# Kernel tuning notes

Hardware: AMD Instinct MI355X
Metric: run time of the kernel (lower is better)

## Reference

```python
import jax, jax.numpy as jnp
import numpy as np

N_NODES = 50000
N_EDGES = 1250000
D_FEAT = 64


def setup_inputs() -> dict:
    key = jax.random.key(0)
    k1, k2, k3, k4 = jax.random.split(key, 4)
    feat = jax.random.normal(k1, (N_NODES, D_FEAT), dtype=jnp.float32)
    edge_weight = jax.random.uniform(k2, (N_EDGES,), dtype=jnp.float32)
    edge_src = jax.random.randint(k3, (N_EDGES,), 0, N_NODES, dtype=jnp.int64)
    edge_dst = jnp.sort(jax.random.randint(k4, (N_EDGES,), 0, N_NODES, dtype=jnp.int64))
    return {"feat": feat, "edge_weight": edge_weight,
            "edge_src": edge_src, "edge_dst": edge_dst}


def reference(feat, edge_weight, edge_src, edge_dst):
    # u_mul_e: gather source node features, scale by per-edge weight
    msgs = feat[edge_src] * edge_weight[:, None]          # [E, d]
    # fn.sum: scatter-add messages to destination nodes
    rst = jax.ops.segment_sum(msgs, edge_dst, num_segments=N_NODES)  # [N, d]
    return rst
```

## Files before the change

kernel.cpp:

```cpp
#include <hip/hip_runtime.h>
#include <hip/hip_fp16.h>

#define D_FEAT 64

__global__ __launch_bounds__(256) void prep_kernel(
    const float* __restrict__ feat, uint2* __restrict__ f16,
    const int* __restrict__ edge_dst, int* __restrict__ rp,
    int n_vec4, int n_edges, int n_nodes, int rb) {
  if ((int)blockIdx.x < rb) {
    const int i = blockIdx.x * blockDim.x + threadIdx.x;
    if (i >= n_vec4) return;
    const float4 v = ((const float4*)feat)[i];
    const __half2 h0 = __float22half2_rn(make_float2(v.x, v.y));
    const __half2 h1 = __float22half2_rn(make_float2(v.z, v.w));
    uint2 o;
    o.x = *(const unsigned int*)&h0;
    o.y = *(const unsigned int*)&h1;
    f16[i] = o;
  } else {
    const int e = (blockIdx.x - rb) * blockDim.x + threadIdx.x;
    if (e > n_edges) return;
    const int d0 = (e == 0) ? -1 : edge_dst[e - 1];
    const int d1 = (e == n_edges) ? n_nodes : edge_dst[e];
    for (int v = d0 + 1; v <= d1; ++v) rp[v] = e;
  }
}

__global__ __launch_bounds__(256) void gcn_gather_f16(
    const uint4* __restrict__ feat16,
    const float* __restrict__ ew,
    const int* __restrict__ esrc,
    const int* __restrict__ rp,
    float* __restrict__ out, int n_nodes) {
  const int total16 = n_nodes * 8;
  const int warm_slices = (total16 + 1023) / 1024;
  const int xcd_seq = blockIdx.x >> 3;
  if (xcd_seq < warm_slices) {
    const int s0 = xcd_seq * 1024;
#pragma unroll
    for (int t = 0; t < 4; ++t) {
      const int idx = s0 + t * 256 + threadIdx.x;
      if (idx < total16) {
        uint4 q = feat16[idx];
        asm volatile("" :: "v"(q.x), "v"(q.y), "v"(q.z), "v"(q.w));
      }
    }
  }

  const int wave = (blockIdx.x * blockDim.x + threadIdx.x) >> 6;
  const int lane = threadIdx.x & 63;
  if (wave >= n_nodes) return;
  const int slot = lane >> 3;
  const int part = lane & 7;

  const int e0 = rp[wave];
  const int e1 = rp[wave + 1];

  float a0 = 0.f, a1 = 0.f, a2 = 0.f, a3 = 0.f;
  float a4 = 0.f, a5 = 0.f, a6 = 0.f, a7 = 0.f;

  for (int base = e0; base < e1; base += 64) {
    const int n = min(64, e1 - base);
    int   s = 0;
    float w = 0.0f;
    if (lane < n) {
      s = esrc[base + lane];
      w = ew[base + lane];
    }
#pragma unroll
    for (int r = 0; r < 8; ++r) {
      const int   sk = __shfl(s, r * 8 + slot);
      const float wk = __shfl(w, r * 8 + slot);
      const uint4 q  = feat16[(size_t)sk * 8 + part];
      const float2 f0 = __half22float2(*(const __half2*)&q.x);
      const float2 f1 = __half22float2(*(const __half2*)&q.y);
      const float2 f2 = __half22float2(*(const __half2*)&q.z);
      const float2 f3 = __half22float2(*(const __half2*)&q.w);
      a0 = fmaf(f0.x, wk, a0); a1 = fmaf(f0.y, wk, a1);
      a2 = fmaf(f1.x, wk, a2); a3 = fmaf(f1.y, wk, a3);
      a4 = fmaf(f2.x, wk, a4); a5 = fmaf(f2.y, wk, a5);
      a6 = fmaf(f3.x, wk, a6); a7 = fmaf(f3.y, wk, a7);
    }
  }

#pragma unroll
  for (int m = 8; m <= 32; m <<= 1) {
    a0 += __shfl_xor(a0, m); a1 += __shfl_xor(a1, m);
    a2 += __shfl_xor(a2, m); a3 += __shfl_xor(a3, m);
    a4 += __shfl_xor(a4, m); a5 += __shfl_xor(a5, m);
    a6 += __shfl_xor(a6, m); a7 += __shfl_xor(a7, m);
  }

  if (slot == 0) {
    float4* orow = (float4*)(out + (size_t)wave * D_FEAT);
    orow[part * 2]     = make_float4(a0, a1, a2, a3);
    orow[part * 2 + 1] = make_float4(a4, a5, a6, a7);
  }
}

extern "C" void kernel_launch(void* const* d_in, const int* in_sizes, int n_in,
                              void* d_out, int out_size, void* d_ws, size_t ws_size,
                              hipStream_t stream) {
  const float* feat        = (const float*)d_in[0];
  const float* edge_weight = (const float*)d_in[1];
  const int*   edge_src    = (const int*)d_in[2];
  const int*   edge_dst    = (const int*)d_in[3];
  float* out = (float*)d_out;

  const int n_edges = in_sizes[1];
  const int n_nodes = out_size / D_FEAT;

  int*   rp  = (int*)d_ws;
  uint2* f16 = (uint2*)((char*)d_ws + (1 << 20));

  const int n_vec4 = n_nodes * (D_FEAT / 4);
  const int rb = (n_vec4 + 255) / 256;
  const int eb = (n_edges + 1 + 255) / 256;
  prep_kernel<<<rb + eb, 256, 0, stream>>>(
      feat, f16, edge_dst, rp, n_vec4, n_edges, n_nodes, rb);

  const long total_threads = (long)n_nodes * 64;
  gcn_gather_f16<<<(int)((total_threads + 255) / 256), 256, 0, stream>>>(
      (const uint4*)f16, edge_weight, edge_src, rp, out, n_nodes);
}
```

Baseline: 110.5 us.

## Split fp16 features into two column halves and gather each in separate passes

The prep kernel now writes the fp16 feature table as two separate arrays, columns 0-31 and 32-63. The gather kernel runs twice, once per half, with 16 edges per wave iteration and 4 lanes per edge. Each pass touches a 3.2MB table instead of 6.4MB, meant to improve cache hit rates for the random source gathers. The cost is reading the edge indices, weights and row pointers twice plus an extra launch. The explicit L2 warm-up prefetch is removed.

```diff
diff --git a/kernel.cpp b/kernel.cpp
--- a/kernel.cpp
+++ b/kernel.cpp
@@ -4,19 +4,24 @@
 #define D_FEAT 64
 
 __global__ __launch_bounds__(256) void prep_kernel(
-    const float* __restrict__ feat, uint2* __restrict__ f16,
+    const float* __restrict__ feat,
+    uint2* __restrict__ fA, uint2* __restrict__ fB,
     const int* __restrict__ edge_dst, int* __restrict__ rp,
-    int n_vec4, int n_edges, int n_nodes, int rb) {
+    int n_nodes, int n_edges, int rb) {
   if ((int)blockIdx.x < rb) {
     const int i = blockIdx.x * blockDim.x + threadIdx.x;
+    const int n_vec4 = n_nodes * 16;
     if (i >= n_vec4) return;
+    const int node = i >> 4;
+    const int c4   = i & 15;
     const float4 v = ((const float4*)feat)[i];
     const __half2 h0 = __float22half2_rn(make_float2(v.x, v.y));
     const __half2 h1 = __float22half2_rn(make_float2(v.z, v.w));
     uint2 o;
     o.x = *(const unsigned int*)&h0;
     o.y = *(const unsigned int*)&h1;
-    f16[i] = o;
+    uint2* dst = (c4 < 8) ? fA : fB;
+    dst[node * 8 + (c4 & 7)] = o;
   } else {
     const int e = (blockIdx.x - rb) * blockDim.x + threadIdx.x;
     if (e > n_edges) return;
@@ -26,32 +31,17 @@
   }
 }
 
-__global__ __launch_bounds__(256) void gcn_gather_f16(
-    const uint4* __restrict__ feat16,
+__global__ __launch_bounds__(256) void gcn_gather_half(
+    const uint4* __restrict__ fh,
     const float* __restrict__ ew,
     const int* __restrict__ esrc,
     const int* __restrict__ rp,
-    float* __restrict__ out, int n_nodes) {
-  const int total16 = n_nodes * 8;
-  const int warm_slices = (total16 + 1023) / 1024;
-  const int xcd_seq = blockIdx.x >> 3;
-  if (xcd_seq < warm_slices) {
-    const int s0 = xcd_seq * 1024;
-#pragma unroll
-    for (int t = 0; t < 4; ++t) {
-      const int idx = s0 + t * 256 + threadIdx.x;
-      if (idx < total16) {
-        uint4 q = feat16[idx];
-        asm volatile("" :: "v"(q.x), "v"(q.y), "v"(q.z), "v"(q.w));
-      }
-    }
-  }
-
+    float* __restrict__ out, int n_nodes, int col_off) {
   const int wave = (blockIdx.x * blockDim.x + threadIdx.x) >> 6;
   const int lane = threadIdx.x & 63;
   if (wave >= n_nodes) return;
-  const int slot = lane >> 3;
-  const int part = lane & 7;
+  const int slot = lane >> 2;
+  const int part = lane & 3;
 
   const int e0 = rp[wave];
   const int e1 = rp[wave + 1];
@@ -68,10 +58,10 @@
       w = ew[base + lane];
     }
 #pragma unroll
-    for (int r = 0; r < 8; ++r) {
-      const int   sk = __shfl(s, r * 8 + slot);
-      const float wk = __shfl(w, r * 8 + slot);
-      const uint4 q  = feat16[(size_t)sk * 8 + part];
+    for (int r = 0; r < 4; ++r) {
+      const int   sk = __shfl(s, r * 16 + slot);
+      const float wk = __shfl(w, r * 16 + slot);
+      const uint4 q  = fh[(size_t)sk * 4 + part];
       const float2 f0 = __half22float2(*(const __half2*)&q.x);
       const float2 f1 = __half22float2(*(const __half2*)&q.y);
       const float2 f2 = __half22float2(*(const __half2*)&q.z);
@@ -84,7 +74,7 @@
   }
 
 #pragma unroll
-  for (int m = 8; m <= 32; m <<= 1) {
+  for (int m = 4; m <= 32; m <<= 1) {
     a0 += __shfl_xor(a0, m); a1 += __shfl_xor(a1, m);
     a2 += __shfl_xor(a2, m); a3 += __shfl_xor(a3, m);
     a4 += __shfl_xor(a4, m); a5 += __shfl_xor(a5, m);
@@ -92,7 +82,7 @@
   }
 
   if (slot == 0) {
-    float4* orow = (float4*)(out + (size_t)wave * D_FEAT);
+    float4* orow = (float4*)(out + (size_t)wave * D_FEAT + col_off);
     orow[part * 2]     = make_float4(a0, a1, a2, a3);
     orow[part * 2 + 1] = make_float4(a4, a5, a6, a7);
   }
@@ -110,16 +100,19 @@
   const int n_edges = in_sizes[1];
   const int n_nodes = out_size / D_FEAT;
 
-  int*   rp  = (int*)d_ws;
-  uint2* f16 = (uint2*)((char*)d_ws + (1 << 20));
+  int*   rp = (int*)d_ws;
+  uint2* fA = (uint2*)((char*)d_ws + (1 << 20));
+  uint2* fB = (uint2*)((char*)d_ws + (1 << 20) + ((size_t)n_nodes * 64));
 
-  const int n_vec4 = n_nodes * (D_FEAT / 4);
+  const int n_vec4 = n_nodes * 16;
   const int rb = (n_vec4 + 255) / 256;
   const int eb = (n_edges + 1 + 255) / 256;
   prep_kernel<<<rb + eb, 256, 0, stream>>>(
-      feat, f16, edge_dst, rp, n_vec4, n_edges, n_nodes, rb);
+      feat, fA, fB, edge_dst, rp, n_nodes, n_edges, rb);
 
-  const long total_threads = (long)n_nodes * 64;
-  gcn_gather_f16<<<(int)((total_threads + 255) / 256), 256, 0, stream>>>(
-      (const uint4*)f16, edge_weight, edge_src, rp, out, n_nodes);
+  const int gblocks = (int)(((long)n_nodes * 64 + 255) / 256);
+  gcn_gather_half<<<gblocks, 256, 0, stream>>>(
+      (const uint4*)fA, edge_weight, edge_src, rp, out, n_nodes, 0);
+  gcn_gather_half<<<gblocks, 256, 0, stream>>>(
+      (const uint4*)fB, edge_weight, edge_src, rp, out, n_nodes, 32);
 }
```

After: 125.2 us. 13.3% more time.
